# Performance work log

Measured on AMD Instinct MI355X. Metric: run time of the kernel, lower is better.

Reference implementation:

```python
import jax, jax.numpy as jnp
import numpy as np

N_STEP = 8
DILATION = 1


def setup_inputs() -> dict:
    key = jax.random.key(0)
    k1, k2 = jax.random.split(key)
    B, C, T, V = 32, 128, 64, 25
    z = jax.random.normal(k1, (B, C, T, V), dtype=jnp.float32)
    W = jax.random.normal(k2, (C, C), dtype=jnp.float32) * 0.02  # channel-mixing ode weight
    b = jnp.zeros((C,), dtype=jnp.float32)
    return {"z": z, "W": W, "b": b}


def reference(z, W, b):
    # z: (B, C, T, V). ode_func acts per-frame on (C, V): linear over channels + tanh.
    B, C, T, V = z.shape

    def ode_func(x):
        # equivalent to applying the C->C linear on the '(b t) c v' layout
        return jnp.tanh(jnp.einsum('bctv,dc->bdtv', x, W) + b[None, :, None, None])

    t_idx = jnp.arange(T)
    z_shift_lst = [z]
    z_lst = [z]
    cur = z
    for i in range(1, N_STEP + 1):
        cur = cur + ode_func(cur)                      # Euler step
        shift = i * DILATION
        # gather with index (arange(T) - shift) % T  ==  circular roll by +shift along T
        rolled = jnp.roll(cur, shift, axis=2)
        mask = (t_idx >= shift)[None, None, :, None]   # zero the first shift frames
        z_shift_lst.append(jnp.where(mask, rolled, jnp.zeros((), cur.dtype)))
        z_lst.append(cur)
    z_shift = jnp.concatenate(z_shift_lst, axis=0)     # ((n_step+1)*B, C, T, V)
    z_cls = jnp.concatenate(z_lst, axis=0)             # ((n_step+1)*B, C, T, V)
    return (z_shift, z_cls)
```

## Files before the change

kernel.cpp:

```cpp
#include <hip/hip_runtime.h>

#define CC     128
#define TT     64
#define VV     25
#define BB     32
#define PP     (TT * VV)
#define CHUNK  (BB * CC * PP)
#define NSTEP  8
#define PTILE  64
#define NPT    (PP / PTILE)

typedef __attribute__((ext_vector_type(8))) __bf16 bf16x8;
typedef __attribute__((ext_vector_type(4))) float  f32x4;

__device__ __forceinline__ float fast_tanh(float x) {
    float e = __expf(2.0f * x);
    return 1.0f - 2.0f * __builtin_amdgcn_rcpf(e + 1.0f);
}

__device__ __forceinline__ void bf16_split(float y, unsigned short& h, unsigned short& lo) {
    unsigned int bits = __float_as_uint(y);
    h = (unsigned short)(bits >> 16);
    float r = y - __uint_as_float(bits & 0xffff0000u);
    lo = (unsigned short)(__float_as_uint(r) >> 16);
}

__device__ __forceinline__ int xb_off(int p, int c) {
    return (p * 256 + c * 2) ^ ((p & 7) << 4) ^ ((p & 8) << 3);
}

__device__ __forceinline__ void lds_barrier() {
    asm volatile("s_waitcnt lgkmcnt(0)" ::: "memory");
    __builtin_amdgcn_sched_barrier(0);
    __builtin_amdgcn_s_barrier();
    __builtin_amdgcn_sched_barrier(0);
}

__global__ __launch_bounds__(256) void euler_fused(
    const float* __restrict__ z, const float* __restrict__ W,
    const float* __restrict__ bias, float* __restrict__ out)
{
    __shared__ unsigned short XH[PTILE * CC];
    __shared__ unsigned short XL[PTILE * CC];

    const int b   = blockIdx.y;
    const int p0  = blockIdx.x * PTILE;
    const int tid = threadIdx.x;
    const int w   = tid >> 6;
    const int lr  = tid & 15;
    const int lh  = (tid >> 4) & 3;

    union BF8 { bf16x8 v; unsigned short u[8]; };
    bf16x8 wh[2][4], wl[2][4];
    #pragma unroll
    for (int dt = 0; dt < 2; ++dt) {
        const int d = (2 * w + dt) * 16 + lr;
        #pragma unroll
        for (int ks = 0; ks < 4; ++ks) {
            const float* wp = W + d * CC + ks * 32 + lh * 8;
            f32x4 f0 = *(const f32x4*)wp;
            f32x4 f1 = *(const f32x4*)(wp + 4);
            BF8 th, tl;
            #pragma unroll
            for (int e = 0; e < 4; ++e) bf16_split(f0[e], th.u[e],     tl.u[e]);
            #pragma unroll
            for (int e = 0; e < 4; ++e) bf16_split(f1[e], th.u[4 + e], tl.u[4 + e]);
            wh[dt][ks] = th.v;
            wl[dt][ks] = tl.v;
        }
    }

    float bv[2][4];
    #pragma unroll
    for (int dt = 0; dt < 2; ++dt)
        #pragma unroll
        for (int j = 0; j < 4; ++j)
            bv[dt][j] = bias[(2 * w + dt) * 16 + lh * 4 + j];

    const float* zb = z + (size_t)b * CC * PP + p0;
    #pragma unroll
    for (int it = 0; it < 8; ++it) {
        int slot = it * 256 + tid;
        int c  = slot >> 4;
        int po = (slot & 15) * 4;
        f32x4 v = *(const f32x4*)(zb + (size_t)c * PP + po);
        size_t o = (size_t)(b * CC + c) * PP + p0 + po;
        *(f32x4*)(out + o)                     = v;
        *(f32x4*)(out + (size_t)9 * CHUNK + o) = v;
        #pragma unroll
        for (int e = 0; e < 4; ++e) {
            unsigned short h, lo;
            bf16_split(v[e], h, lo);
            int off = xb_off(po + e, c);
            *(unsigned short*)((char*)XH + off) = h;
            *(unsigned short*)((char*)XL + off) = lo;
        }
    }

    float st[4][2][4];
    #pragma unroll
    for (int pt = 0; pt < 4; ++pt)
        #pragma unroll
        for (int dt = 0; dt < 2; ++dt)
            #pragma unroll
            for (int j = 0; j < 4; ++j)
                st[pt][dt][j] =
                    z[(size_t)(b * CC + (2 * w + dt) * 16 + lh * 4 + j) * PP + p0 + pt * 16 + lr];

    lds_barrier();

    const int swz = ((lr & 7) << 4) ^ ((lr & 8) << 3);

    #pragma unroll
    for (int i = 1; i <= NSTEP; ++i) {
        f32x4 acc[4][2];
        #pragma unroll
        for (int pt = 0; pt < 4; ++pt)
            #pragma unroll
            for (int dt = 0; dt < 2; ++dt)
                acc[pt][dt] = (f32x4){0.0f, 0.0f, 0.0f, 0.0f};

        #pragma unroll
        for (int pt = 0; pt < 4; ++pt) {
            #pragma unroll
            for (int ks = 0; ks < 4; ++ks) {
                const int ro = ((pt * 16 + lr) * 256 + ks * 64 + lh * 16) ^ swz;
                bf16x8 bh = *(const bf16x8*)((const char*)XH + ro);
                bf16x8 bl = *(const bf16x8*)((const char*)XL + ro);
                #pragma unroll
                for (int dt = 0; dt < 2; ++dt) {
                    acc[pt][dt] = __builtin_amdgcn_mfma_f32_16x16x32_bf16(wh[dt][ks], bh, acc[pt][dt], 0, 0, 0);
                    acc[pt][dt] = __builtin_amdgcn_mfma_f32_16x16x32_bf16(wh[dt][ks], bl, acc[pt][dt], 0, 0, 0);
                    acc[pt][dt] = __builtin_amdgcn_mfma_f32_16x16x32_bf16(wl[dt][ks], bh, acc[pt][dt], 0, 0, 0);
                }
            }
        }

        #pragma unroll
        for (int pt = 0; pt < 4; ++pt)
            #pragma unroll
            for (int dt = 0; dt < 2; ++dt)
                #pragma unroll
                for (int j = 0; j < 4; ++j)
                    st[pt][dt][j] += fast_tanh(acc[pt][dt][j] + bv[dt][j]);

        if (i < NSTEP) {
            lds_barrier();

            #pragma unroll
            for (int pt = 0; pt < 4; ++pt)
                #pragma unroll
                for (int dt = 0; dt < 2; ++dt) {
                    ushort4 hv, lv;
                    bf16_split(st[pt][dt][0], hv.x, lv.x);
                    bf16_split(st[pt][dt][1], hv.y, lv.y);
                    bf16_split(st[pt][dt][2], hv.z, lv.z);
                    bf16_split(st[pt][dt][3], hv.w, lv.w);
                    const int off = xb_off(pt * 16 + lr, (2 * w + dt) * 16 + lh * 4);
                    *(ushort4*)((char*)XH + off) = hv;
                    *(ushort4*)((char*)XL + off) = lv;
                }

            lds_barrier();
        }

        const size_t shiftBase = (size_t)i * CHUNK;
        const size_t clsBase   = (size_t)(9 + i) * CHUNK;
        const int s = VV * i;
        const bool fast = (p0 >= s) && (p0 + PTILE - 1 + s < PP);
        #pragma unroll
        for (int pt = 0; pt < 4; ++pt) {
            const int p = p0 + pt * 16 + lr;
            #pragma unroll
            for (int dt = 0; dt < 2; ++dt) {
                #pragma unroll
                for (int j = 0; j < 4; ++j) {
                    const int d = (2 * w + dt) * 16 + lh * 4 + j;
                    const size_t row = (size_t)(b * CC + d) * PP;
                    const float y = st[pt][dt][j];
                    out[clsBase + row + p] = y;
                    if (fast) {
                        out[shiftBase + row + p + s] = y;
                    } else {
                        const int q = p + s;
                        if (q < PP) out[shiftBase + row + q] = y;
                        if (p < s)  out[shiftBase + row + p] = 0.0f;
                    }
                }
            }
        }
    }
}

extern "C" void kernel_launch(void* const* d_in, const int* in_sizes, int n_in,
                              void* d_out, int out_size, void* d_ws, size_t ws_size,
                              hipStream_t stream) {
    const float* z    = (const float*)d_in[0];
    const float* W    = (const float*)d_in[1];
    const float* bias = (const float*)d_in[2];
    float* out = (float*)d_out;

    hipLaunchKernelGGL(euler_fused, dim3(NPT, BB), dim3(256), 0, stream, z, W, bias, out);
}
```

Baseline: 589.6 us.

## Enlarge point tile to 160 and keep Euler state in LDS split-bf16

Raises the per-block point tile from 64 to 160, so each block reuses its weight fragments over more points and the grid shrinks to 320 blocks. The separate fp32 state array is dropped: each step rebuilds the previous state from the hi/lo bf16 pair already in LDS and adds the tanh term into the accumulators. The step loop is no longer unrolled, and the launch bounds now ask for two blocks per SM. The aim is to free registers and amortise weight loads. The cost is about 80KB of LDS per block and uneven load across CUs. Rebuilding the state from two bf16 halves also drops low mantissa bits, and that error compounds over the Euler steps.

```diff
diff --git a/kernel.cpp b/kernel.cpp
--- a/kernel.cpp
+++ b/kernel.cpp
@@ -7,7 +7,7 @@
 #define PP     (TT * VV)
 #define CHUNK  (BB * CC * PP)
 #define NSTEP  8
-#define PTILE  64
+#define PTILE  160
 #define NPT    (PP / PTILE)
 
 typedef __attribute__((ext_vector_type(8))) __bf16 bf16x8;
@@ -25,6 +25,10 @@
     lo = (unsigned short)(__float_as_uint(r) >> 16);
 }
 
+__device__ __forceinline__ float bf16_up(unsigned short u) {
+    return __uint_as_float(((unsigned int)u) << 16);
+}
+
 __device__ __forceinline__ int xb_off(int p, int c) {
     return (p * 256 + c * 2) ^ ((p & 7) << 4) ^ ((p & 8) << 3);
 }
@@ -36,7 +40,7 @@
     __builtin_amdgcn_sched_barrier(0);
 }
 
-__global__ __launch_bounds__(256) void euler_fused(
+__global__ __launch_bounds__(256, 2) void euler_fused(
     const float* __restrict__ z, const float* __restrict__ W,
     const float* __restrict__ bias, float* __restrict__ out)
 {
@@ -79,10 +83,10 @@
 
     const float* zb = z + (size_t)b * CC * PP + p0;
     #pragma unroll
-    for (int it = 0; it < 8; ++it) {
-        int slot = it * 256 + tid;
-        int c  = slot >> 4;
-        int po = (slot & 15) * 4;
+    for (int it = 0; it < 20; ++it) {
+        unsigned int slot = it * 256 + tid;
+        unsigned int c  = slot / 40;
+        unsigned int po = (slot % 40) * 4;
         f32x4 v = *(const f32x4*)(zb + (size_t)c * PP + po);
         size_t o = (size_t)(b * CC + c) * PP + p0 + po;
         *(f32x4*)(out + o)                     = v;
@@ -97,31 +101,21 @@
         }
     }
 
-    float st[4][2][4];
-    #pragma unroll
-    for (int pt = 0; pt < 4; ++pt)
-        #pragma unroll
-        for (int dt = 0; dt < 2; ++dt)
-            #pragma unroll
-            for (int j = 0; j < 4; ++j)
-                st[pt][dt][j] =
-                    z[(size_t)(b * CC + (2 * w + dt) * 16 + lh * 4 + j) * PP + p0 + pt * 16 + lr];
-
     lds_barrier();
 
     const int swz = ((lr & 7) << 4) ^ ((lr & 8) << 3);
 
-    #pragma unroll
+    #pragma unroll 1
     for (int i = 1; i <= NSTEP; ++i) {
-        f32x4 acc[4][2];
-        #pragma unroll
-        for (int pt = 0; pt < 4; ++pt)
+        f32x4 acc[10][2];
+        #pragma unroll
+        for (int pt = 0; pt < 10; ++pt)
             #pragma unroll
             for (int dt = 0; dt < 2; ++dt)
                 acc[pt][dt] = (f32x4){0.0f, 0.0f, 0.0f, 0.0f};
 
         #pragma unroll
-        for (int pt = 0; pt < 4; ++pt) {
+        for (int pt = 0; pt < 10; ++pt) {
             #pragma unroll
             for (int ks = 0; ks < 4; ++ks) {
                 const int ro = ((pt * 16 + lr) * 256 + ks * 64 + lh * 16) ^ swz;
@@ -137,25 +131,33 @@
         }
 
         #pragma unroll
-        for (int pt = 0; pt < 4; ++pt)
-            #pragma unroll
-            for (int dt = 0; dt < 2; ++dt)
-                #pragma unroll
-                for (int j = 0; j < 4; ++j)
-                    st[pt][dt][j] += fast_tanh(acc[pt][dt][j] + bv[dt][j]);
+        for (int pt = 0; pt < 10; ++pt)
+            #pragma unroll
+            for (int dt = 0; dt < 2; ++dt) {
+                const int off = xb_off(pt * 16 + lr, (2 * w + dt) * 16 + lh * 4);
+                ushort4 h4 = *(const ushort4*)((const char*)XH + off);
+                ushort4 l4 = *(const ushort4*)((const char*)XL + off);
+                const unsigned short hu[4] = {h4.x, h4.y, h4.z, h4.w};
+                const unsigned short lu[4] = {l4.x, l4.y, l4.z, l4.w};
+                #pragma unroll
+                for (int j = 0; j < 4; ++j) {
+                    float xo = bf16_up(hu[j]) + bf16_up(lu[j]);
+                    acc[pt][dt][j] = xo + fast_tanh(acc[pt][dt][j] + bv[dt][j]);
+                }
+            }
 
         if (i < NSTEP) {
             lds_barrier();
 
             #pragma unroll
-            for (int pt = 0; pt < 4; ++pt)
+            for (int pt = 0; pt < 10; ++pt)
                 #pragma unroll
                 for (int dt = 0; dt < 2; ++dt) {
                     ushort4 hv, lv;
-                    bf16_split(st[pt][dt][0], hv.x, lv.x);
-                    bf16_split(st[pt][dt][1], hv.y, lv.y);
-                    bf16_split(st[pt][dt][2], hv.z, lv.z);
-                    bf16_split(st[pt][dt][3], hv.w, lv.w);
+                    bf16_split(acc[pt][dt][0], hv.x, lv.x);
+                    bf16_split(acc[pt][dt][1], hv.y, lv.y);
+                    bf16_split(acc[pt][dt][2], hv.z, lv.z);
+                    bf16_split(acc[pt][dt][3], hv.w, lv.w);
                     const int off = xb_off(pt * 16 + lr, (2 * w + dt) * 16 + lh * 4);
                     *(ushort4*)((char*)XH + off) = hv;
                     *(ushort4*)((char*)XL + off) = lv;
@@ -167,9 +169,9 @@
         const size_t shiftBase = (size_t)i * CHUNK;
         const size_t clsBase   = (size_t)(9 + i) * CHUNK;
         const int s = VV * i;
-        const bool fast = (p0 >= s) && (p0 + PTILE - 1 + s < PP);
-        #pragma unroll
-        for (int pt = 0; pt < 4; ++pt) {
+        const bool fast = (p0 >= s) && (p0 + PTILE + s <= PP);
+        #pragma unroll
+        for (int pt = 0; pt < 10; ++pt) {
             const int p = p0 + pt * 16 + lr;
             #pragma unroll
             for (int dt = 0; dt < 2; ++dt) {
@@ -177,7 +179,7 @@
                 for (int j = 0; j < 4; ++j) {
                     const int d = (2 * w + dt) * 16 + lh * 4 + j;
                     const size_t row = (size_t)(b * CC + d) * PP;
-                    const float y = st[pt][dt][j];
+                    const float y = acc[pt][dt][j];
                     out[clsBase + row + p] = y;
                     if (fast) {
                         out[shiftBase + row + p + s] = y;
```

Measured after the change: 670.7 us. 13.8% more time.
